# Optimization experiments

Measured on AMD Instinct MI355X. Metric: run time of the kernel, lower is better.

Reference implementation:

```python
import jax, jax.numpy as jnp
import numpy as np
from jax import lax

EPS_COS = 1e-8  # torch F.cosine_similarity eps
EPS_GN = 1e-5   # torch GroupNorm eps


def setup_inputs() -> dict:
    key = jax.random.key(0)
    k1, k2, k3 = jax.random.split(key, 3)
    b, f, h, w = 4, 64, 64, 64
    fdm = jax.random.uniform(k1, (b, 1, 2 * h, 2 * w), dtype=jnp.float32)
    x = jax.random.normal(k2, (b, f, h, w), dtype=jnp.float32)
    W_fuse = jax.random.normal(k3, (f, 2 * f, 3, 3), dtype=jnp.float32) * 0.05
    b_fuse = jnp.zeros((f,), jnp.float32)
    gamma = jnp.ones((f,), jnp.float32)
    beta = jnp.zeros((f,), jnp.float32)
    return {"fdm": fdm, "x": x, "W_fuse": W_fuse, "b_fuse": b_fuse,
            "gamma": gamma, "beta": beta}


def reference(fdm, x, W_fuse, b_fuse, gamma, beta):
    b, f, h, w = x.shape
    # adaptive_max_pool2d(fdm, (h, w)): input spatial is exact multiple -> plain max pool
    kh, kw = fdm.shape[2] // h, fdm.shape[3] // w
    fdm_p = lax.reduce_window(fdm, -jnp.inf, lax.max,
                              (1, 1, kh, kw), (1, 1, kh, kw), 'VALID')  # [b,1,h,w]
    # per-sample threshold: min(0.5, max(fdm)/3)
    maxv = jnp.max(fdm_p, axis=(1, 2, 3))                 # [b]
    thre = jnp.minimum(0.5, maxv / 3.0)                   # [b]
    mask = fdm_p.reshape(b, h * w) >= thre[:, None]       # [b, HW] selected pixels

    # cosine similarity between selected feature vectors and all positions.
    # Original masked-selects N rows then computes N x HW sims and max-reduces over N;
    # we compute the full HW x HW sim and mask unselected rows to -inf (same max).
    xf = x.reshape(b, f, h * w).transpose(0, 2, 1)        # [b, HW, f]
    norm = jnp.sqrt(jnp.sum(xf * xf, axis=-1, keepdims=True))
    xn = xf / jnp.maximum(norm, EPS_COS)
    sim = jnp.einsum('bpf,bqf->bpq', xn, xn)              # [b, HW(sel), HW(all)]
    sim = jnp.where(mask[:, :, None], sim, -jnp.inf)
    sm = (jnp.max(sim, axis=1) / 2.0 + 0.5).reshape(b, 1, h, w)

    # fuse: Conv2d(2f -> f, k3, pad1) + GroupNorm(1, f) + ReLU
    cat = jnp.concatenate([sm * x, x], axis=1)            # [b, 2f, h, w]
    y = lax.conv_general_dilated(cat, W_fuse, (1, 1), 'SAME',
                                 dimension_numbers=('NCHW', 'OIHW', 'NCHW'))
    y = y + b_fuse[None, :, None, None]
    mu = jnp.mean(y, axis=(1, 2, 3), keepdims=True)
    var = jnp.mean((y - mu) ** 2, axis=(1, 2, 3), keepdims=True)
    y = (y - mu) / jnp.sqrt(var + EPS_GN)
    y = y * gamma[None, :, None, None] + beta[None, :, None, None]
    x0 = jax.nn.relu(y)
    return x0, sm
```

## Files before the change

kernel.cpp:

```cpp
#include <hip/hip_runtime.h>
#include <math.h>


#define HW 4096
#define NCH 64

typedef __attribute__((ext_vector_type(8))) short short8;
typedef __attribute__((ext_vector_type(4))) float f32x4;

static __device__ __forceinline__ ushort f2bf(float f) {
    unsigned u = __float_as_uint(f);
    unsigned r = (u + 0x7fffu + ((u >> 16) & 1u)) >> 16;
    return (ushort)r;
}
static __device__ __forceinline__ float bf2f(ushort h) {
    return __uint_as_float(((unsigned)h) << 16);
}
static __device__ __forceinline__ unsigned mapf(float f) {
    unsigned u = __float_as_uint(f);
    return u ^ ((unsigned)((int)u >> 31) | 0x80000000u);
}
static __device__ __forceinline__ float unmapf(unsigned u) {
    unsigned b = (u & 0x80000000u) ? (u ^ 0x80000000u) : ~u;
    return __uint_as_float(b);
}
static __device__ __forceinline__ void gl2lds(const void* g, void* l) {
    __builtin_amdgcn_global_load_lds((const __attribute__((address_space(1))) void*)g,
                                     (__attribute__((address_space(3))) void*)l, 16, 0, 0);
}

__global__ __launch_bounds__(256) void k_pnp(
    const float* __restrict__ fdm, const float* __restrict__ x, const float* __restrict__ W,
    float* __restrict__ pooledOut, float* __restrict__ threOut,
    int* __restrict__ unsel, int* __restrict__ unselN, unsigned* __restrict__ scores,
    float* __restrict__ gnS1, float* __restrict__ gnS2,
    float* __restrict__ rn, float* __restrict__ smOut, ushort* __restrict__ inb,
    ushort* __restrict__ wbh, ushort* __restrict__ wbl, uint4* __restrict__ zpage) {
    const int t = threadIdx.x;
    if (blockIdx.x < 4) {
        const int b = blockIdx.x;
        __shared__ float pooled[4096];
        __shared__ float red[256];
        __shared__ int cnt;
        const float* fb = fdm + b * 16384;
        float lmax = -1.0f;
#pragma unroll
        for (int it = 0; it < 8; ++it) {
            int id2 = it * 256 + t;
            int i = id2 >> 5;
            int j2 = id2 & 31;
            const float* base = fb + i * 256 + j2 * 4;
            float4 a = *(const float4*)base;
            float4 c = *(const float4*)(base + 128);
            float p0 = fmaxf(fmaxf(a.x, a.y), fmaxf(c.x, c.y));
            float p1 = fmaxf(fmaxf(a.z, a.w), fmaxf(c.z, c.w));
            pooled[i * 64 + j2 * 2]     = p0;
            pooled[i * 64 + j2 * 2 + 1] = p1;
            lmax = fmaxf(lmax, fmaxf(p0, p1));
        }
        red[t] = lmax;
        __syncthreads();
        for (int s = 128; s > 0; s >>= 1) {
            if (t < s) red[t] = fmaxf(red[t], red[t + s]);
            __syncthreads();
        }
        __shared__ float thre_s;
        if (t == 0) {
            thre_s = fminf(0.5f, red[0] / 3.0f);
            cnt = 0;
            gnS1[b] = 0.0f; gnS2[b] = 0.0f;
            if (b == 0) *zpage = make_uint4(0u, 0u, 0u, 0u);
        }
        __syncthreads();
        const float th = thre_s;
#pragma unroll
        for (int it = 0; it < 4; ++it) {
            int idx = (it * 256 + t) * 4;
            *(float4*)(pooledOut + b * 4096 + idx) = *(const float4*)(pooled + idx);
        }
        for (int idx = t; idx < 4096; idx += 256) {
            scores[b * 4096 + idx] = 0u;
            if (!(pooled[idx] >= th)) {
                int pos = atomicAdd(&cnt, 1);
                unsel[b * 4096 + pos] = idx;
            }
        }
        __syncthreads();
        if (t == 0) { unselN[b] = cnt; threOut[b] = th; }
    } else if (blockIdx.x < 260) {
        __shared__ float s_part[4][64];
        const int n = blockIdx.x - 4;
        const int b = n >> 6;
        const int pbase = (n & 63) * 64;
        const int wv = t >> 6;
        const int l = t & 63;
        const int sp = pbase + l;
        const float* xp = x + b * (NCH * HW) + sp;
        float xv[16];
        float ss = 0.f;
#pragma unroll
        for (int i = 0; i < 16; ++i) {
            float a = xp[(wv * 16 + i) * HW];
            xv[i] = a;
            ss += a * a;
        }
        s_part[wv][l] = ss;
        ushort h[16];
#pragma unroll
        for (int i = 0; i < 16; ++i) h[i] = f2bf(xv[i]);
        size_t dst1 = ((size_t)(b * 8 + wv) * 4096 + sp) * 16;
        size_t dst2 = ((size_t)(b * 8 + 4 + wv) * 4096 + sp) * 16;
        *(uint4*)(inb + dst1)     = *(const uint4*)h;
        *(uint4*)(inb + dst1 + 8) = *(const uint4*)(h + 8);
        *(uint4*)(inb + dst2)     = *(const uint4*)h;
        *(uint4*)(inb + dst2 + 8) = *(const uint4*)(h + 8);
        __syncthreads();
        if (t < 64) {
            float s = s_part[0][l] + s_part[1][l] + s_part[2][l] + s_part[3][l];
            int g = b * HW + pbase + l;
            rn[g] = 1.0f / fmaxf(sqrtf(s), 1e-8f);
            smOut[g] = 1.0f;
        }
    } else {
        const int u = (blockIdx.x - 260) * 256 + t;
        const int tap = u >> 10;
        const int rem = u & 1023;
        const int oc = rem >> 4;
        const int g = rem & 15;
        ushort hh[8], ll[8];
#pragma unroll
        for (int j = 0; j < 8; ++j) {
            int ic = g * 8 + j;
            float v = W[(oc * 128 + ic) * 9 + tap];
            ushort hb = f2bf(v);
            hh[j] = hb;
            ll[j] = f2bf(v - bf2f(hb));
        }
        *(uint4*)(wbh + (size_t)u * 8) = *(const uint4*)hh;
        *(uint4*)(wbl + (size_t)u * 8) = *(const uint4*)ll;
    }
}

__global__ __launch_bounds__(256) void k_score(
    const float* __restrict__ rn, const float* __restrict__ pooledM, const float* __restrict__ threArr,
    const int* __restrict__ unsel, const int* __restrict__ unselN,
    const ushort* __restrict__ inb, unsigned* __restrict__ scores) {
    const int b = blockIdx.y;
    const int n0 = blockIdx.x * 128;
    const int t = threadIdx.x;
    const int lane = t & 63;
    const int wave = t >> 6;
    const int li = lane & 15;
    const int quad = lane >> 4;
    const int nu = unselN[b];
    if (nu == 0) return;

    __shared__ __align__(16) ushort s_qh[64 * 72];
    __shared__ __align__(16) ushort s_ql[64 * 72];
    __shared__ unsigned s_best[64];

    const float th = threArr[b];
    const int p0 = n0 + (2 * wave) * 16 + li;
    const int p1 = n0 + (2 * wave + 1) * 16 + li;
    const float rp0 = rn[b * 4096 + p0];
    const float rp1 = rn[b * 4096 + p1];
    const float ng0 = (pooledM[b * 4096 + p0] >= th) ? 0.0f : -INFINITY;
    const float ng1 = (pooledM[b * 4096 + p1] >= th) ? 0.0f : -INFINITY;

    for (int qs0 = 0; qs0 < nu; qs0 += 64) {
        __syncthreads();
        for (int idx = t; idx < 512; idx += 256) {
            int q_l = idx >> 3;
            int part = idx & 7;
            int qg = qs0 + q_l;
            int q = 0;
            float rq = 0.0f;
            if (qg < nu) {
                q = unsel[b * 4096 + qg];
                rq = rn[b * 4096 + q];
            }
            uint4 raw = *(const uint4*)(inb + (((size_t)(b * 8 + 4 + (part >> 1)) * 4096) + q) * 16 + (part & 1) * 8);
            ushort hv[8]; *(uint4*)hv = raw;
            ushort hh[8], ll[8];
#pragma unroll
            for (int j = 0; j < 8; ++j) {
                float v = bf2f(hv[j]) * rq;
                hh[j] = f2bf(v);
                ll[j] = f2bf(v - bf2f(hh[j]));
            }
            int c0 = (part >> 1) * 16 + (part & 1) * 8;
            *(uint4*)(s_qh + q_l * 72 + c0) = *(const uint4*)hh;
            *(uint4*)(s_ql + q_l * 72 + c0) = *(const uint4*)ll;
        }
        if (t < 64) s_best[t] = 0u;
        __syncthreads();

        f32x4 acc[2][4];
#pragma unroll
        for (int nt = 0; nt < 2; ++nt)
#pragma unroll
            for (int mt = 0; mt < 4; ++mt) acc[nt][mt] = (f32x4){0.f, 0.f, 0.f, 0.f};
#pragma unroll
        for (int k0 = 0; k0 < 2; ++k0) {
            const int cb = k0 * 32 + quad * 8;
            const int grp = 4 + (cb >> 4);
            const int sub = cb & 15;
            short8 b0 = *(const short8*)(inb + (((size_t)(b * 8 + grp) * 4096) + p0) * 16 + sub);
            short8 b1 = *(const short8*)(inb + (((size_t)(b * 8 + grp) * 4096) + p1) * 16 + sub);
#pragma unroll
            for (int mt = 0; mt < 4; ++mt) {
                short8 ah = *(const short8*)(s_qh + (size_t)(mt * 16 + li) * 72 + cb);
                short8 al = *(const short8*)(s_ql + (size_t)(mt * 16 + li) * 72 + cb);
                acc[0][mt] = __builtin_amdgcn_mfma_f32_16x16x32_bf16(ah, b0, acc[0][mt], 0, 0, 0);
                acc[0][mt] = __builtin_amdgcn_mfma_f32_16x16x32_bf16(al, b0, acc[0][mt], 0, 0, 0);
                acc[1][mt] = __builtin_amdgcn_mfma_f32_16x16x32_bf16(ah, b1, acc[1][mt], 0, 0, 0);
                acc[1][mt] = __builtin_amdgcn_mfma_f32_16x16x32_bf16(al, b1, acc[1][mt], 0, 0, 0);
            }
        }
#pragma unroll
        for (int mt = 0; mt < 4; ++mt) {
#pragma unroll
            for (int r = 0; r < 4; ++r) {
                float sc = fmaxf(acc[0][mt][r] * rp0 + ng0, acc[1][mt][r] * rp1 + ng1);
                sc = fmaxf(sc, __shfl_xor(sc, 1));
                sc = fmaxf(sc, __shfl_xor(sc, 2));
                sc = fmaxf(sc, __shfl_xor(sc, 4));
                sc = fmaxf(sc, __shfl_xor(sc, 8));
                if (li == 0) atomicMax(&s_best[mt * 16 + quad * 4 + r], mapf(sc));
            }
        }
        __syncthreads();
        if (t < 64 && qs0 + t < nu) atomicMax(scores + b * 4096 + qs0 + t, s_best[t]);
    }
}

__global__ __launch_bounds__(256) void k_conv_mfma(
    const ushort* __restrict__ inb, const ushort* __restrict__ wbh, const ushort* __restrict__ wbl,
    const float* __restrict__ bfuse, const int* __restrict__ unsel, const int* __restrict__ unselN,
    const unsigned* __restrict__ scores, float* __restrict__ smOut, const uint4* __restrict__ zpage,
    float* __restrict__ y, float* __restrict__ gnS1, float* __restrict__ gnS2) {
    const int rowblk = blockIdx.x;
    const int ocblk = blockIdx.y;
    const int b = blockIdx.z;
    const int t = threadIdx.x;
    const int lane = t & 63;
    const int wave = t >> 6;
    const int li = lane & 15;
    const int quad = lane >> 4;
    const int h0 = rowblk * 4;
    const int oc0 = ocblk * 16;
    const int nu = unselN[b];

    __shared__ __align__(16) ushort s_in[2][4 * 396 * 8];
    __shared__ __align__(16) ushort s_w[2][4 * 288 * 8];
    __shared__ float red1[256];
    __shared__ float red2[256];

    if (rowblk == 0 && ocblk == 0) {
        for (int qi = t; qi < nu; qi += 256) {
            float sm = unmapf(scores[b * 4096 + qi]) * 0.5f + 0.5f;
            smOut[b * 4096 + unsel[b * 4096 + qi]] = sm;
        }
    }

    f32x4 acc[4];
#pragma unroll
    for (int j = 0; j < 4; ++j) acc[j] = (f32x4){0.f, 0.f, 0.f, 0.f};

    auto issue = [&](int chunk, int buf) {
        const int part = wave;
        const int grp = 2 * chunk + (part >> 1);
        const int sub = (part & 1) * 8;
        const ushort* gbase = inb + (((size_t)(b * 8 + grp)) * 4096) * 16 + sub;
        ushort* lin = &s_in[buf][part * 3168];
#pragma unroll
        for (int i = 0; i < 7; ++i) {
            int cell = i * 64 + lane;
            if (cell < 396) {
                int r = cell / 66;
                int c = cell - r * 66;
                int h = h0 + r - 1;
                int w = c - 1;
                bool ok = ((unsigned)h < 64u) && ((unsigned)w < 64u);
                const void* src = ok ? (const void*)(gbase + (size_t)(h * 64 + w) * 16) : (const void*)zpage;
                gl2lds(src, lin + i * 512);
            }
        }
        const int ic0 = chunk * 32;
        ushort* lw = &s_w[buf][part * 2304];
#pragma unroll
        for (int i = 0; i < 5; ++i) {
            int j = i * 64 + lane;
            if (j < 288) {
                int hl = (j >= 144);
                int e = j - hl * 144;
                int tap = e >> 4;
                int o = e & 15;
                const ushort* src = (hl ? wbl : wbh) + ((size_t)(tap * 64 + oc0 + o) * 128 + ic0 + part * 8);
                gl2lds(src, lw + i * 512);
            }
        }
    };

    issue(2, 0);

    for (int a = 0; a < 4; ++a) {
        const int chunk = a ^ 2;
        const int buf = a & 1;
        __syncthreads();
        if (chunk < 2) {
            for (int idx = t; idx < nu * 4; idx += 256) {
                int qi = idx >> 2;
                int part = idx & 3;
                int q = unsel[b * 4096 + qi];
                int hq = q >> 6, wq = q & 63;
                int r = hq - h0 + 1;
                if ((unsigned)r < 6u) {
                    float sm = unmapf(scores[b * 4096 + qi]) * 0.5f + 0.5f;
                    ushort* ptr = &s_in[buf][part * 3168 + (r * 66 + wq + 1) * 8];
                    ushort hv[8];
                    *(uint4*)hv = *(const uint4*)ptr;
#pragma unroll
                    for (int j = 0; j < 8; ++j) hv[j] = f2bf(bf2f(hv[j]) * sm);
                    *(uint4*)ptr = *(const uint4*)hv;
                }
            }
            __syncthreads();
        }
        if (a < 3) issue((a + 1) ^ 2, 1 - buf);
        {
            const ushort* sin = &s_in[buf][quad * 3168];
            const ushort* swq = &s_w[buf][quad * 2304];
#pragma unroll
            for (int kh = 0; kh < 3; ++kh) {
                const int r = wave + kh;
#pragma unroll
                for (int kw = 0; kw < 3; ++kw) {
                    const int tap = kh * 3 + kw;
                    short8 ah = *(const short8*)(swq + (tap * 16 + li) * 8);
                    short8 al = *(const short8*)(swq + 1152 + (tap * 16 + li) * 8);
#pragma unroll
                    for (int j = 0; j < 4; ++j) {
                        int c = j * 16 + li + kw;
                        short8 bv = *(const short8*)(sin + (r * 66 + c) * 8);
                        acc[j] = __builtin_amdgcn_mfma_f32_16x16x32_bf16(ah, bv, acc[j], 0, 0, 0);
                        acc[j] = __builtin_amdgcn_mfma_f32_16x16x32_bf16(al, bv, acc[j], 0, 0, 0);
                    }
                }
            }
        }
    }
    float bias[4];
#pragma unroll
    for (int reg = 0; reg < 4; ++reg) bias[reg] = bfuse[oc0 + quad * 4 + reg];
    float s1 = 0.f, s2 = 0.f;
    const int hrow = h0 + wave;
#pragma unroll
    for (int j = 0; j < 4; ++j) {
#pragma unroll
        for (int reg = 0; reg < 4; ++reg) {
            float v = acc[j][reg] + bias[reg];
            y[((size_t)(b * 64 + oc0 + quad * 4 + reg)) * HW + hrow * 64 + j * 16 + li] = v;
            s1 += v; s2 += v * v;
        }
    }
    red1[t] = s1; red2[t] = s2;
    __syncthreads();
    for (int s = 128; s > 0; s >>= 1) {
        if (t < s) { red1[t] += red1[t + s]; red2[t] += red2[t + s]; }
        __syncthreads();
    }
    if (t == 0) {
        atomicAdd(&gnS1[b], red1[0]);
        atomicAdd(&gnS2[b], red2[0]);
    }
}

__global__ void k_gn(float* __restrict__ out, const float* __restrict__ gnS1, const float* __restrict__ gnS2,
                     const float* __restrict__ gamma, const float* __restrict__ beta) {
    const int e = (blockIdx.x * 256 + threadIdx.x) * 4;
    const int b = e >> 18;
    const int c = (e >> 12) & 63;
    const float inv = 1.0f / 262144.0f;
    float mu = gnS1[b] * inv;
    float var = gnS2[b] * inv - mu * mu;
    float rs = rsqrtf(var + 1e-5f);
    float scale = rs * gamma[c];
    float shift = beta[c] - mu * scale;
    float4 v = *(const float4*)(out + e);
    float4 o;
    o.x = fmaxf(v.x * scale + shift, 0.0f);
    o.y = fmaxf(v.y * scale + shift, 0.0f);
    o.z = fmaxf(v.z * scale + shift, 0.0f);
    o.w = fmaxf(v.w * scale + shift, 0.0f);
    *(float4*)(out + e) = o;
}

extern "C" void kernel_launch(void* const* d_in, const int* in_sizes, int n_in,
                              void* d_out, int out_size, void* d_ws, size_t ws_size,
                              hipStream_t stream) {
    const float* fdm   = (const float*)d_in[0];
    const float* x     = (const float*)d_in[1];
    const float* Wf    = (const float*)d_in[2];
    const float* bfuse = (const float*)d_in[3];
    const float* gamma = (const float*)d_in[4];
    const float* beta  = (const float*)d_in[5];
    float* out = (float*)d_out;
    float* ws  = (float*)d_ws;

    float*    rn      = ws;
    float*    pooledM = rn + 16384;
    int*      unsel   = (int*)(pooledM + 16384);
    unsigned* scores  = (unsigned*)(unsel + 16384);
    float*    thre    = (float*)(scores + 16384);
    int*      unselN  = (int*)(thre + 4);
    float*    gnS1    = (float*)(unselN + 4);
    float*    gnS2    = gnS1 + 4;
    uint4*    zpage   = (uint4*)(gnS2 + 4);
    ushort*   wbh     = (ushort*)(zpage + 1);
    ushort*   wbl     = wbh + 73728;
    ushort*   inb     = wbl + 73728;

    float* yout  = out;
    float* smOut = out + 1048576;

    k_pnp<<<dim3(296), dim3(256), 0, stream>>>(fdm, x, Wf, pooledM, thre, unsel, unselN,
                                               scores, gnS1, gnS2, rn, smOut, inb, wbh, wbl, zpage);
    k_score<<<dim3(32, 4), dim3(256), 0, stream>>>(rn, pooledM, thre, unsel, unselN, inb, scores);
    k_conv_mfma<<<dim3(16, 4, 4), dim3(256), 0, stream>>>(inb, wbh, wbl, bfuse, unsel, unselN,
                                                          scores, smOut, zpage, yout, gnS1, gnS2);
    k_gn<<<dim3(1024), dim3(256), 0, stream>>>(yout, gnS1, gnS2, gamma, beta);
}
```

Baseline: 99.98 us.

## Fuse GroupNorm+ReLU into conv kernel via per-batch grid barrier

Removes the separate GroupNorm kernel and the round trip of conv output through global memory. Each conv block adds its partial sums, increments a per-batch counter, and spins until all 64 blocks of that batch have arrived. It then applies normalization and ReLU to the accumulators still in registers before writing the output. This relies on all 256 blocks being co-resident, which holds for this grid size on this GPU, and adds spin-wait latency.

```diff
diff --git a/kernel.cpp b/kernel.cpp
--- a/kernel.cpp
+++ b/kernel.cpp
@@ -33,7 +33,7 @@
     const float* __restrict__ fdm, const float* __restrict__ x, const float* __restrict__ W,
     float* __restrict__ pooledOut, float* __restrict__ threOut,
     int* __restrict__ unsel, int* __restrict__ unselN, unsigned* __restrict__ scores,
-    float* __restrict__ gnS1, float* __restrict__ gnS2,
+    float* __restrict__ gnS1, float* __restrict__ gnS2, int* __restrict__ gnCnt,
     float* __restrict__ rn, float* __restrict__ smOut, ushort* __restrict__ inb,
     ushort* __restrict__ wbh, ushort* __restrict__ wbl, uint4* __restrict__ zpage) {
     const int t = threadIdx.x;
@@ -68,7 +68,7 @@
         if (t == 0) {
             thre_s = fminf(0.5f, red[0] / 3.0f);
             cnt = 0;
-            gnS1[b] = 0.0f; gnS2[b] = 0.0f;
+            gnS1[b] = 0.0f; gnS2[b] = 0.0f; gnCnt[b] = 0;
             if (b == 0) *zpage = make_uint4(0u, 0u, 0u, 0u);
         }
         __syncthreads();
@@ -236,9 +236,10 @@
 
 __global__ __launch_bounds__(256) void k_conv_mfma(
     const ushort* __restrict__ inb, const ushort* __restrict__ wbh, const ushort* __restrict__ wbl,
-    const float* __restrict__ bfuse, const int* __restrict__ unsel, const int* __restrict__ unselN,
+    const float* __restrict__ bfuse, const float* __restrict__ gamma, const float* __restrict__ beta,
+    const int* __restrict__ unsel, const int* __restrict__ unselN,
     const unsigned* __restrict__ scores, float* __restrict__ smOut, const uint4* __restrict__ zpage,
-    float* __restrict__ y, float* __restrict__ gnS1, float* __restrict__ gnS2) {
+    float* __restrict__ out, float* __restrict__ gnS1, float* __restrict__ gnS2, int* __restrict__ gnCnt) {
     const int rowblk = blockIdx.x;
     const int ocblk = blockIdx.y;
     const int b = blockIdx.z;
@@ -255,6 +256,7 @@
     __shared__ __align__(16) ushort s_w[2][4 * 288 * 8];
     __shared__ float red1[256];
     __shared__ float red2[256];
+    __shared__ float s_mu, s_rs;
 
     if (rowblk == 0 && ocblk == 0) {
         for (int qi = t; qi < nu; qi += 256) {
@@ -354,13 +356,11 @@
 #pragma unroll
     for (int reg = 0; reg < 4; ++reg) bias[reg] = bfuse[oc0 + quad * 4 + reg];
     float s1 = 0.f, s2 = 0.f;
-    const int hrow = h0 + wave;
 #pragma unroll
     for (int j = 0; j < 4; ++j) {
 #pragma unroll
         for (int reg = 0; reg < 4; ++reg) {
             float v = acc[j][reg] + bias[reg];
-            y[((size_t)(b * 64 + oc0 + quad * 4 + reg)) * HW + hrow * 64 + j * 16 + li] = v;
             s1 += v; s2 += v * v;
         }
     }
@@ -373,27 +373,34 @@
     if (t == 0) {
         atomicAdd(&gnS1[b], red1[0]);
         atomicAdd(&gnS2[b], red2[0]);
-    }
-}
-
-__global__ void k_gn(float* __restrict__ out, const float* __restrict__ gnS1, const float* __restrict__ gnS2,
-                     const float* __restrict__ gamma, const float* __restrict__ beta) {
-    const int e = (blockIdx.x * 256 + threadIdx.x) * 4;
-    const int b = e >> 18;
-    const int c = (e >> 12) & 63;
-    const float inv = 1.0f / 262144.0f;
-    float mu = gnS1[b] * inv;
-    float var = gnS2[b] * inv - mu * mu;
-    float rs = rsqrtf(var + 1e-5f);
-    float scale = rs * gamma[c];
-    float shift = beta[c] - mu * scale;
-    float4 v = *(const float4*)(out + e);
-    float4 o;
-    o.x = fmaxf(v.x * scale + shift, 0.0f);
-    o.y = fmaxf(v.y * scale + shift, 0.0f);
-    o.z = fmaxf(v.z * scale + shift, 0.0f);
-    o.w = fmaxf(v.w * scale + shift, 0.0f);
-    *(float4*)(out + e) = o;
+        __threadfence();
+        atomicAdd(&gnCnt[b], 1);
+        while (__hip_atomic_load(&gnCnt[b], __ATOMIC_RELAXED, __HIP_MEMORY_SCOPE_AGENT) < 64) {
+            __builtin_amdgcn_s_sleep(8);
+        }
+        __threadfence();
+        float S1 = __hip_atomic_load(&gnS1[b], __ATOMIC_RELAXED, __HIP_MEMORY_SCOPE_AGENT);
+        float S2 = __hip_atomic_load(&gnS2[b], __ATOMIC_RELAXED, __HIP_MEMORY_SCOPE_AGENT);
+        const float inv = 1.0f / 262144.0f;
+        float mu = S1 * inv;
+        float var = S2 * inv - mu * mu;
+        s_mu = mu;
+        s_rs = rsqrtf(var + 1e-5f);
+    }
+    __syncthreads();
+    const float mu = s_mu, rs = s_rs;
+    const int hrow = h0 + wave;
+#pragma unroll
+    for (int reg = 0; reg < 4; ++reg) {
+        const int oc = oc0 + quad * 4 + reg;
+        const float scale = rs * gamma[oc];
+        const float shift = beta[oc] - mu * scale;
+#pragma unroll
+        for (int j = 0; j < 4; ++j) {
+            float v = acc[j][reg] + bias[reg];
+            out[((size_t)(b * 64 + oc)) * HW + hrow * 64 + j * 16 + li] = fmaxf(v * scale + shift, 0.0f);
+        }
+    }
 }
 
 extern "C" void kernel_launch(void* const* d_in, const int* in_sizes, int n_in,
@@ -416,18 +423,18 @@
     int*      unselN  = (int*)(thre + 4);
     float*    gnS1    = (float*)(unselN + 4);
     float*    gnS2    = gnS1 + 4;
-    uint4*    zpage   = (uint4*)(gnS2 + 4);
+    int*      gnCnt   = (int*)(gnS2 + 4);
+    uint4*    zpage   = (uint4*)(gnCnt + 4);
     ushort*   wbh     = (ushort*)(zpage + 1);
     ushort*   wbl     = wbh + 73728;
     ushort*   inb     = wbl + 73728;
 
-    float* yout  = out;
     float* smOut = out + 1048576;
 
     k_pnp<<<dim3(296), dim3(256), 0, stream>>>(fdm, x, Wf, pooledM, thre, unsel, unselN,
-                                               scores, gnS1, gnS2, rn, smOut, inb, wbh, wbl, zpage);
+                                               scores, gnS1, gnS2, gnCnt, rn, smOut, inb, wbh, wbl, zpage);
     k_score<<<dim3(32, 4), dim3(256), 0, stream>>>(rn, pooledM, thre, unsel, unselN, inb, scores);
-    k_conv_mfma<<<dim3(16, 4, 4), dim3(256), 0, stream>>>(inb, wbh, wbl, bfuse, unsel, unselN,
-                                                          scores, smOut, zpage, yout, gnS1, gnS2);
-    k_gn<<<dim3(1024), dim3(256), 0, stream>>>(yout, gnS1, gnS2, gamma, beta);
-}
+    k_conv_mfma<<<dim3(16, 4, 4), dim3(256), 0, stream>>>(inb, wbh, wbl, bfuse, gamma, beta,
+                                                          unsel, unselN, scores, smOut, zpage,
+                                                          out, gnS1, gnS2, gnCnt);
+}
```

Measured after the change: 108.8 us. 8.8% more time.
